# Performance work log

Measured on AMD Instinct MI355X. Metric: run time of the kernel, lower is better.

## Reference

```python
import jax, jax.numpy as jnp
import numpy as np

B, S, D, H, L, F = 2, 2048, 512, 8, 6, 2048
MAX = 5000
HD = D // H
OFF = MAX - 1


def _layernorm(x, g, b, eps=1e-5):
    m = jnp.mean(x, axis=-1, keepdims=True)
    v = jnp.mean((x - m) ** 2, axis=-1, keepdims=True)
    return (x - m) / jnp.sqrt(v + eps) * g + b


def _sinusoidal_pe(seq_len, d_model):
    pos = jnp.arange(seq_len, dtype=jnp.float32)[:, None]
    div = jnp.exp(jnp.arange(0, d_model, 2, dtype=jnp.float32) * (-np.log(10000.0) / d_model))
    pe = jnp.zeros((seq_len, d_model), jnp.float32)
    pe = pe.at[:, 0::2].set(jnp.sin(pos * div))
    pe = pe.at[:, 1::2].set(jnp.cos(pos * div))
    return pe


def setup_inputs() -> dict:
    key = jax.random.key(0)
    ks = iter(jax.random.split(key, 64))

    def n(shape, s):
        return (jax.random.normal(next(ks), shape, jnp.float32) * s).astype(jnp.float32)

    inp = {}
    inp['x'] = jax.random.normal(next(ks), (B, S, D), jnp.float32)
    inp['f0'] = jax.random.normal(next(ks), (B, S, 1), jnp.float32)
    inp['sp'] = jax.random.normal(next(ks), (B, S, 1), jnp.float32)
    inp['ap'] = jax.random.normal(next(ks), (B, S, 1), jnp.float32)
    inp['spk_emb'] = jax.random.normal(next(ks), (B, D), jnp.float32)
    # conditional positional encoding projections (weights stored as (in,out); y = x @ W + b)
    inp['Wf0'] = n((1, D), 0.1); inp['bf0'] = jnp.zeros((D,), jnp.float32)
    inp['Wsp'] = n((1, D), 0.1); inp['bsp'] = jnp.zeros((D,), jnp.float32)
    inp['Wap'] = n((1, D), 0.1); inp['bap'] = jnp.zeros((D,), jnp.float32)
    inp['Wspk'] = n((D, D), 0.02); inp['bspk'] = jnp.zeros((D,), jnp.float32)
    # per-layer stacked params
    inp['Wq'] = n((L, D, D), 0.02); inp['bq'] = jnp.zeros((L, D), jnp.float32)
    inp['Wk'] = n((L, D, D), 0.02); inp['bk'] = jnp.zeros((L, D), jnp.float32)
    inp['Wv'] = n((L, D, D), 0.02); inp['bv'] = jnp.zeros((L, D), jnp.float32)
    inp['Wo'] = n((L, D, D), 0.02); inp['bo'] = jnp.zeros((L, D), jnp.float32)
    inp['ln1_g'] = jnp.ones((L, D), jnp.float32); inp['ln1_b'] = jnp.zeros((L, D), jnp.float32)
    inp['ln2_g'] = jnp.ones((L, D), jnp.float32); inp['ln2_b'] = jnp.zeros((L, D), jnp.float32)
    inp['W1'] = n((L, D, F), 0.02); inp['b1'] = jnp.zeros((L, F), jnp.float32)
    inp['W2'] = n((L, F, D), 0.02); inp['b2'] = jnp.zeros((L, D), jnp.float32)
    inp['rel_table'] = n((L, 2 * MAX - 1, H), 0.02)
    inp['gfin'] = jnp.ones((D,), jnp.float32); inp['bfin'] = jnp.zeros((D,), jnp.float32)
    return inp


def _forward(x, f0, sp, ap, spk_emb,
             Wf0, bf0, Wsp, bsp, Wap, bap, Wspk, bspk,
             Wq, bq, Wk, bk, Wv, bv, Wo, bo,
             ln1_g, ln1_b, ln2_g, ln2_b, W1, b1, W2, b2,
             rel_table, gfin, bfin):
    # --- conditional positional encoding (dropout = identity, eval mode) ---
    x = x + _sinusoidal_pe(S, D)[None]
    x = x + (f0 @ Wf0 + bf0)
    x = x + (sp @ Wsp + bsp)
    x = x + (ap @ Wap + bap)
    spk = jnp.broadcast_to(spk_emb[:, None, :], (B, S, D))
    x = x + (spk @ Wspk + bspk)

    # relative coords: added bias for (query q, key k) is table[k - q + OFF] (matches transpose(1,3) in torch)
    coords = jnp.arange(S)
    rel = jnp.clip(coords[None, :] - coords[:, None] + OFF, 0, 2 * MAX - 2)  # (S_q, S_k)

    scale = 1.0 / np.sqrt(HD)

    def layer(x, p):
        (Wq_, bq_, Wk_, bk_, Wv_, bv_, Wo_, bo_,
         g1, be1, g2, be2, W1_, b1_, W2_, b2_, tab) = p
        res = x
        h = _layernorm(x, g1, be1)
        Q = (h @ Wq_ + bq_).reshape(B, S, H, HD)
        K = (h @ Wk_ + bk_).reshape(B, S, H, HD)
        V = (h @ Wv_ + bv_).reshape(B, S, H, HD)
        scores = jnp.einsum('bqhd,bkhd->bhqk', Q, K) * scale
        bias = jnp.transpose(tab[rel], (2, 0, 1))  # (H, S_q, S_k)
        scores = scores + bias[None]
        attn = jax.nn.softmax(scores, axis=-1)
        ao = jnp.einsum('bhqk,bkhd->bqhd', attn, V).reshape(B, S, D)
        x = res + (ao @ Wo_ + bo_)
        res = x
        h = _layernorm(x, g2, be2)
        h = jax.nn.gelu(h @ W1_ + b1_, approximate=False)
        x = res + (h @ W2_ + b2_)
        return x, None

    params = (Wq, bq, Wk, bk, Wv, bv, Wo, bo,
              ln1_g, ln1_b, ln2_g, ln2_b, W1, b1, W2, b2, rel_table)
    x, _ = jax.lax.scan(layer, x, params)
    return _layernorm(x, gfin, bfin)


def reference(x, f0, sp, ap, spk_emb,
              Wf0, bf0, Wsp, bsp, Wap, bap, Wspk, bspk,
              Wq, bq, Wk, bk, Wv, bv, Wo, bo,
              ln1_g, ln1_b, ln2_g, ln2_b, W1, b1, W2, b2,
              rel_table, gfin, bfin):
    return _forward(x, f0, sp, ap, spk_emb,
                    Wf0, bf0, Wsp, bsp, Wap, bap, Wspk, bspk,
                    Wq, bq, Wk, bk, Wv, bv, Wo, bo,
                    ln1_g, ln1_b, ln2_g, ln2_b, W1, b1, W2, b2,
                    rel_table, gfin, bfin)
```

## Files before the change

kernel.cpp:

```cpp
#include <hip/hip_runtime.h>
#include <hip/hip_bf16.h>

#define B_ 2
#define S_ 2048
#define D_ 512
#define H_ 8
#define L_ 6
#define F_ 2048
#define HD_ 64
#define M_ 4096
#define OFF_ 4999
#define NREL_ 9999

typedef short s8v __attribute__((ext_vector_type(8)));
typedef float f4v __attribute__((ext_vector_type(4)));

enum { MODE_BF16 = 0, MODE_RES = 1, MODE_GELU = 2 };

__device__ __forceinline__ short f2bf(float f) {
  unsigned u = __float_as_uint(f);
  unsigned r = (u + 0x7fffu + ((u >> 16) & 1u)) >> 16;
  return (short)r;
}

__device__ __forceinline__ float exp2fast(float x) {
  float r;
  asm("v_exp_f32 %0, %1" : "=v"(r) : "v"(x));
  return r;
}

__device__ __forceinline__ void gload16(const void* g, const void* l) {
  __builtin_amdgcn_global_load_lds((const __attribute__((address_space(1))) unsigned int*)g,
                                   (__attribute__((address_space(3))) unsigned int*)l,
                                   16, 0, 0);
}

__global__ void transpose_kernel(const float* __restrict__ src, short* __restrict__ dst,
                                 int K, int N, long srcBS, long dstBS, int rowOff)
{
  __shared__ float t[32][33];
  int tx = threadIdx.x, ty = threadIdx.y;
  int n0 = blockIdx.x * 32, k0 = blockIdx.y * 32, l = blockIdx.z;
  const float* s = src + (size_t)l * srcBS;
  short* d = dst + (size_t)l * dstBS;
  for (int j = 0; j < 4; ++j)
    t[ty + j*8][tx] = s[(size_t)(k0 + ty + j*8) * N + n0 + tx];
  __syncthreads();
  for (int j = 0; j < 4; ++j)
    d[(size_t)(rowOff + n0 + ty + j*8) * K + k0 + tx] = f2bf(t[tx][ty + j*8]);
}

__global__ void packb_kernel(const float* __restrict__ bq, const float* __restrict__ bk,
                             const float* __restrict__ bv, float* __restrict__ bqkv)
{
  int i = blockIdx.x * 256 + threadIdx.x;
  if (i >= L_ * 1536) return;
  int l = i / 1536, j = i % 1536;
  float v = (j < 512) ? bq[l*512 + j] : (j < 1024) ? bk[l*512 + j - 512] : bv[l*512 + j - 1024];
  bqkv[i] = v;
}

__global__ void tabt_kernel(const float* __restrict__ tab, float* __restrict__ tabT)
{
  int i = blockIdx.x * 256 + threadIdx.x;
  if (i >= L_ * H_ * NREL_) return;
  int l = i / (H_ * NREL_), rem = i % (H_ * NREL_);
  int h = rem / NREL_, idx = rem % NREL_;
  tabT[i] = tab[((size_t)l * NREL_ + idx) * H_ + h] * 1.44269504f;
}

__global__ __launch_bounds__(256) void spk_kernel(const float* __restrict__ spk,
                                                  const float* __restrict__ Wspk,
                                                  const float* __restrict__ bspk,
                                                  float* __restrict__ sproj)
{
  __shared__ float red[4][64];
  int b = blockIdx.x, nb = blockIdx.y;
  int dl = threadIdx.x & 63, kc = threadIdx.x >> 6;
  int d = nb * 64 + dl;
  const float* sprow = spk + b * D_;
  float a0 = 0.f, a1 = 0.f;
  int kbeg = kc * 128;
  for (int k = kbeg; k < kbeg + 128; k += 2) {
    a0 += sprow[k]     * Wspk[(size_t)k * D_ + d];
    a1 += sprow[k + 1] * Wspk[(size_t)(k + 1) * D_ + d];
  }
  red[kc][dl] = a0 + a1;
  __syncthreads();
  if (kc == 0)
    sproj[b*D_ + d] = red[0][dl] + red[1][dl] + red[2][dl] + red[3][dl] + bspk[d];
}

__global__ __launch_bounds__(256) void prologue_kernel(
    const float* __restrict__ x, const float* __restrict__ f0, const float* __restrict__ sp,
    const float* __restrict__ ap, const float* __restrict__ Wf0, const float* __restrict__ bf0,
    const float* __restrict__ Wsp, const float* __restrict__ bsp,
    const float* __restrict__ Wap, const float* __restrict__ bap,
    const float* __restrict__ sproj, float* __restrict__ X)
{
  int row = blockIdx.x, tid = threadIdx.x;
  int b = row >> 11, s = row & 2047;
  float vf0 = f0[row], vsp = sp[row], vap = ap[row];
  for (int j = 0; j < 2; ++j) {
    int d = tid + j * 256;
    int i = d >> 1;
    float div = expf((float)(2*i) * -0.01798894603f);
    float arg = (float)s * div;
    float pe = (d & 1) ? cosf(arg) : sinf(arg);
    float v = x[(size_t)row*D_ + d] + pe
            + vf0*Wf0[d] + bf0[d] + vsp*Wsp[d] + bsp[d] + vap*Wap[d] + bap[d]
            + sproj[b*D_ + d];
    X[(size_t)row*D_ + d] = v;
  }
}

__global__ __launch_bounds__(256) void ln_kernel(
    const float* __restrict__ X, const float* __restrict__ g, const float* __restrict__ bta,
    short* __restrict__ outB, float* __restrict__ outF, int f32out)
{
  __shared__ float red[8];
  int row = blockIdx.x, tid = threadIdx.x;
  const float* xr = X + (size_t)row * D_;
  float v0 = xr[tid], v1 = xr[tid + 256];
  float s = v0 + v1, q = v0*v0 + v1*v1;
  for (int off = 1; off < 64; off <<= 1) { s += __shfl_xor(s, off); q += __shfl_xor(q, off); }
  int w = tid >> 6;
  if ((tid & 63) == 0) { red[w*2] = s; red[w*2 + 1] = q; }
  __syncthreads();
  s = red[0] + red[2] + red[4] + red[6];
  q = red[1] + red[3] + red[5] + red[7];
  float mean = s * (1.0f / D_);
  float var = q * (1.0f / D_) - mean * mean;
  float rstd = rsqrtf(var + 1e-5f);
  float o0 = (v0 - mean) * rstd * g[tid] + bta[tid];
  float o1 = (v1 - mean) * rstd * g[tid + 256] + bta[tid + 256];
  if (f32out) {
    outF[(size_t)row*D_ + tid] = o0; outF[(size_t)row*D_ + tid + 256] = o1;
  } else {
    outB[(size_t)row*D_ + tid] = f2bf(o0); outB[(size_t)row*D_ + tid + 256] = f2bf(o1);
  }
}

template<int MODE>
__device__ __forceinline__ void gemm_body(
    const short* __restrict__ A, const short* __restrict__ Wt,
    const float* __restrict__ bias, int K, int N,
    float* outF, short* outB)
{
  __shared__ short sA[2][4096];
  __shared__ short sB[2][2048];
  const int tid = threadIdx.x;
  const int w = tid >> 6, lane = tid & 63;
  const int col = lane & 15, quad = lane >> 4;
  const int m0 = blockIdx.x * 128, n0 = blockIdx.y * 64;
  const int z = blockIdx.z;
  const int Ksub = K / gridDim.z;
  const int kbase = z * Ksub;
  const int nkt = Ksub >> 6;

  const int rowT = tid >> 2, kcA = tid & 3;
  const size_t kc8 = kcA * 8;

  f4v acc[2][4] = {};
  for (int kt = 0; kt < nkt; ++kt) {
    const int k0 = kbase + kt * 64;
    __syncthreads();
    for (int p = 0; p < 2; ++p) {
      gload16(A + (size_t)(m0 + rowT) * K + k0 + p*32 + kc8,       &sA[p][(w*16) * 32]);
      gload16(A + (size_t)(m0 + 64 + rowT) * K + k0 + p*32 + kc8,  &sA[p][(64 + w*16) * 32]);
      gload16(Wt + (size_t)(n0 + rowT) * K + k0 + p*32 + kc8,      &sB[p][(w*16) * 32]);
    }
    __syncthreads();
    for (int p = 0; p < 2; ++p) {
      s8v af[2], bfr[4];
      for (int mt = 0; mt < 2; ++mt)
        af[mt] = *(const s8v*)&sA[p][(w*32 + mt*16 + col) * 32 + quad * 8];
      for (int nt = 0; nt < 4; ++nt)
        bfr[nt] = *(const s8v*)&sB[p][(nt*16 + col) * 32 + quad * 8];
      for (int mt = 0; mt < 2; ++mt)
        for (int nt = 0; nt < 4; ++nt)
          acc[mt][nt] = __builtin_amdgcn_mfma_f32_16x16x32_bf16(af[mt], bfr[nt], acc[mt][nt], 0, 0, 0);
    }
  }

  const float qsc = (MODE == MODE_BF16 && n0 < 512) ? 0.18033688f : 1.0f;
  float bz[4];
  for (int nt = 0; nt < 4; ++nt)
    bz[nt] = (z == 0) ? bias[n0 + nt*16 + col] : 0.0f;
  for (int mt = 0; mt < 2; ++mt) {
    int mbase = m0 + w*32 + mt*16 + quad*4;
    for (int nt = 0; nt < 4; ++nt) {
      int n = n0 + nt*16 + col;
      for (int r = 0; r < 4; ++r) {
        float v = acc[mt][nt][r] + bz[nt];
        size_t idx = (size_t)(mbase + r) * N + n;
        if (MODE == MODE_RES) {
          atomicAdd(outF + idx, v);
        } else if (MODE == MODE_GELU) {
          outB[idx] = f2bf(0.5f * v * (1.0f + erff(v * 0.70710678118f)));
        } else {
          outB[idx] = f2bf(v * qsc);
        }
      }
    }
  }
}

__global__ __launch_bounds__(256) void gemm_qkv_kernel(
    const short* __restrict__ A, const short* __restrict__ Wt,
    const float* __restrict__ bias, float* outF, short* outB)
{ gemm_body<MODE_BF16>(A, Wt, bias, 512, 1536, outF, outB); }

__global__ __launch_bounds__(256) void gemm_o_kernel(
    const short* __restrict__ A, const short* __restrict__ Wt,
    const float* __restrict__ bias, float* outF, short* outB)
{ gemm_body<MODE_RES>(A, Wt, bias, 512, 512, outF, outB); }

__global__ __launch_bounds__(256) void gemm_ffn1_kernel(
    const short* __restrict__ A, const short* __restrict__ Wt,
    const float* __restrict__ bias, float* outF, short* outB)
{ gemm_body<MODE_GELU>(A, Wt, bias, 512, 2048, outF, outB); }

__global__ __launch_bounds__(256) void gemm_ffn2_kernel(
    const short* __restrict__ A, const short* __restrict__ Wt,
    const float* __restrict__ bias, float* outF, short* outB)
{ gemm_body<MODE_RES>(A, Wt, bias, 2048, 512, outF, outB); }

__global__ __launch_bounds__(256) void vtrans_kernel(const short* __restrict__ QKV,
                                                     short* __restrict__ Vt)
{
  __shared__ short t[64 * 72];
  int tid = threadIdx.x;
  int s0 = blockIdx.x * 64, bh = blockIdx.y;
  int b = bh >> 3, h = bh & 7;
  for (int it = 0; it < 2; ++it) {
    int c = it * 256 + tid;
    int sR = c >> 3, hc = c & 7;
    s8v v = *(const s8v*)(QKV + (size_t)(b*S_ + s0 + sR) * 1536 + 1024 + h*64 + hc*8);
    *(s8v*)&t[sR * 72 + hc * 8] = v;
  }
  __syncthreads();
  for (int it = 0; it < 2; ++it) {
    int c = it * 256 + tid;
    int hd = c >> 3, sc = c & 7;
    s8v v;
    for (int j = 0; j < 8; ++j) v[j] = t[(sc*8 + j) * 72 + hd];
    *(s8v*)(Vt + (size_t)(bh*64 + hd) * S_ + s0 + sc*8) = v;
  }
}

__global__ __launch_bounds__(512) void flash_kernel(
    const short* __restrict__ QKV, const short* __restrict__ Vt,
    const float* __restrict__ tabT, short* __restrict__ AO)
{
  __shared__ __attribute__((aligned(16))) short sQ[2 * 128 * 40];
  __shared__ __attribute__((aligned(16))) short sK[2 * 2 * 32 * 40];
  __shared__ __attribute__((aligned(16))) short sV[2 * 64 * 40];
  __shared__ __attribute__((aligned(16))) short sP[8 * 2 * 16 * 40];
  __shared__ float sBias[192];
  __shared__ float sRow[8 * 16];

  const int tid = threadIdx.x;
  const int w = tid >> 6, lane = tid & 63;
  const int col = lane & 15, quad = lane >> 4;
  const int bh = blockIdx.x, qt = blockIdx.y;
  const int b = bh >> 3, h = bh & 7;
  const int q0 = qt * 128;
  const int wq = w * 16;
  const int nkt = S_ / 64;
  const float* tabh = tabT + (size_t)h * NREL_;

  for (int j = 0; j < 2; ++j) {
    int Lc = j * 512 + tid;
    int c4q = Lc & 3, q = (Lc >> 2) & 127, hc = Lc >> 9;
    *(int4*)&sQ[hc*5120 + q*40 + c4q*8] =
      *(const int4*)(QKV + (size_t)(b*S_ + q0 + q) * 1536 + h*64 + hc*32 + c4q*8);
  }

  const int c4 = tid & 3;
  const int kK = (tid >> 2) & 63, hcK = tid >> 8;
  const short* gK = QKV + (size_t)(b*S_ + kK) * 1536 + 512 + h*64 + hcK*32 + c4*8;
  short* dK = &sK[(kK >> 5)*2560 + hcK*1280 + (kK & 31)*40 + c4*8];
  const int c8 = tid & 7, hdV = tid >> 3;
  const short* gV = Vt + (size_t)(bh*64 + hdV) * S_ + c8*8;
  short* dV = &sV[(c8 >> 2)*2560 + hdV*40 + (c8 & 3)*8];

  int4 rk = *(const int4*)gK;
  int4 rv = *(const int4*)gV;
  float rbias = (tid < 192) ? tabh[0 - q0 - 127 + OFF_ + tid] : 0.0f;

  s8v bQ[2];
  float lsum = 0.0f;
  f4v o[4] = {};

  for (int kt = 0; kt < nkt; ++kt) {
    __syncthreads();
    *(int4*)dK = rk;
    *(int4*)dV = rv;
    if (tid < 192) sBias[tid] = rbias;
    __syncthreads();
    if (kt == 0) {
      bQ[0] = *(const s8v*)&sQ[0*5120 + (wq + col)*40 + quad*8];
      bQ[1] = *(const s8v*)&sQ[1*5120 + (wq + col)*40 + quad*8];
    }
    if (kt + 1 < nkt) {
      rk = *(const int4*)(gK + (size_t)(kt + 1) * 64 * 1536);
      rv = *(const int4*)(gV + (kt + 1) * 64);
      if (tid < 192) rbias = tabh[(kt + 1)*64 - q0 - 127 + OFF_ + tid];
    }

    for (int ko = 0; ko < 2; ++ko) {
      f4v st[2] = {};
      for (int mt = 0; mt < 2; ++mt) {
        s8v aK0 = *(const s8v*)&sK[ko*2560 + 0*1280 + (mt*16 + col)*40 + quad*8];
        s8v aK1 = *(const s8v*)&sK[ko*2560 + 1*1280 + (mt*16 + col)*40 + quad*8];
        st[mt] = __builtin_amdgcn_mfma_f32_16x16x32_bf16(aK0, bQ[0], st[mt], 0, 0, 0);
        st[mt] = __builtin_amdgcn_mfma_f32_16x16x32_bf16(aK1, bQ[1], st[mt], 0, 0, 0);
      }
      for (int mt = 0; mt < 2; ++mt) {
        int ib0 = ko*32 + mt*16 + quad*4 + 127 - wq - col;
        float p0 = exp2fast(st[mt][0] + sBias[ib0 + 0]);
        float p1 = exp2fast(st[mt][1] + sBias[ib0 + 1]);
        float p2 = exp2fast(st[mt][2] + sBias[ib0 + 2]);
        float p3 = exp2fast(st[mt][3] + sBias[ib0 + 3]);
        lsum += (p0 + p1) + (p2 + p3);
        unsigned u0 = __float_as_uint(p0) + 0x8000u;
        unsigned u1 = __float_as_uint(p1) + 0x8000u;
        unsigned u2 = __float_as_uint(p2) + 0x8000u;
        unsigned u3 = __float_as_uint(p3) + 0x8000u;
        int2 pk;
        pk.x = (int)((u0 >> 16) | (u1 & 0xffff0000u));
        pk.y = (int)((u2 >> 16) | (u3 & 0xffff0000u));
        *(int2*)&sP[w*1280 + ko*640 + col*40 + mt*16 + quad*4] = pk;
      }
      s8v aP = *(const s8v*)&sP[w*1280 + ko*640 + col*40 + quad*8];
      for (int nt = 0; nt < 4; ++nt) {
        s8v bv = *(const s8v*)&sV[ko*2560 + (nt*16 + col)*40 + quad*8];
        o[nt] = __builtin_amdgcn_mfma_f32_16x16x32_bf16(aP, bv, o[nt], 0, 0, 0);
      }
    }
  }

  lsum += __shfl_xor(lsum, 16);
  lsum += __shfl_xor(lsum, 32);
  if (lane < 16) sRow[w*16 + lane] = lsum;
  float rs[4];
  for (int r = 0; r < 4; ++r) rs[r] = sRow[w*16 + quad*4 + r];
  for (int nt = 0; nt < 4; ++nt)
    for (int r = 0; r < 4; ++r) {
      float v = o[nt][r] / rs[r];
      size_t m = (size_t)(b*S_ + q0 + wq + quad*4 + r);
      AO[m * 512 + h*64 + nt*16 + col] = f2bf(v);
    }
}

extern "C" void kernel_launch(void* const* d_in, const int* in_sizes, int n_in,
                              void* d_out, int out_size, void* d_ws, size_t ws_size,
                              hipStream_t stream)
{
  const float* x    = (const float*)d_in[0];
  const float* f0   = (const float*)d_in[1];
  const float* sp   = (const float*)d_in[2];
  const float* ap   = (const float*)d_in[3];
  const float* spk  = (const float*)d_in[4];
  const float* Wf0  = (const float*)d_in[5];  const float* bf0  = (const float*)d_in[6];
  const float* Wsp  = (const float*)d_in[7];  const float* bsp  = (const float*)d_in[8];
  const float* Wap  = (const float*)d_in[9];  const float* bap  = (const float*)d_in[10];
  const float* Wspk = (const float*)d_in[11]; const float* bspk = (const float*)d_in[12];
  const float* Wq   = (const float*)d_in[13]; const float* bq   = (const float*)d_in[14];
  const float* Wk   = (const float*)d_in[15]; const float* bk   = (const float*)d_in[16];
  const float* Wv   = (const float*)d_in[17]; const float* bv   = (const float*)d_in[18];
  const float* Wo   = (const float*)d_in[19]; const float* bo   = (const float*)d_in[20];
  const float* ln1g = (const float*)d_in[21]; const float* ln1b = (const float*)d_in[22];
  const float* ln2g = (const float*)d_in[23]; const float* ln2b = (const float*)d_in[24];
  const float* W1   = (const float*)d_in[25]; const float* b1   = (const float*)d_in[26];
  const float* W2   = (const float*)d_in[27]; const float* b2   = (const float*)d_in[28];
  const float* tab  = (const float*)d_in[29];
  const float* gfin = (const float*)d_in[30]; const float* bfin = (const float*)d_in[31];

  char* p = (char*)d_ws;
  auto alloc = [&](size_t bytes) { char* r = p; p += (bytes + 255) & ~(size_t)255; return r; };
  short* WqkvT = (short*)alloc((size_t)L_ * 1536 * 512 * 2);
  short* WoT   = (short*)alloc((size_t)L_ * 512 * 512 * 2);
  short* W1T   = (short*)alloc((size_t)L_ * 2048 * 512 * 2);
  short* W2T   = (short*)alloc((size_t)L_ * 512 * 2048 * 2);
  float* bqkv  = (float*)alloc((size_t)L_ * 1536 * 4);
  float* X     = (float*)alloc((size_t)M_ * D_ * 4);
  short* Hb    = (short*)alloc((size_t)M_ * D_ * 2);
  short* AO    = (short*)alloc((size_t)M_ * D_ * 2);
  short* QKVb  = (short*)alloc((size_t)M_ * 1536 * 2);
  short* VtG   = (short*)alloc((size_t)B_ * H_ * HD_ * S_ * 2);
  short* H1b   = QKVb;
  float* sproj = (float*)alloc((size_t)B_ * D_ * 4);
  float* tabT  = (float*)alloc((size_t)L_ * H_ * NREL_ * 4);

  dim3 b256(256);
  dim3 tb(32, 8);
  packb_kernel<<<dim3((L_*1536 + 255)/256), b256, 0, stream>>>(bq, bk, bv, bqkv);
  tabt_kernel<<<dim3((L_*H_*NREL_ + 255)/256), b256, 0, stream>>>(tab, tabT);
  transpose_kernel<<<dim3(16, 16, L_), tb, 0, stream>>>(Wq, WqkvT, 512, 512, 512*512, 1536*512, 0);
  transpose_kernel<<<dim3(16, 16, L_), tb, 0, stream>>>(Wk, WqkvT, 512, 512, 512*512, 1536*512, 512);
  transpose_kernel<<<dim3(16, 16, L_), tb, 0, stream>>>(Wv, WqkvT, 512, 512, 512*512, 1536*512, 1024);
  transpose_kernel<<<dim3(16, 16, L_), tb, 0, stream>>>(Wo, WoT, 512, 512, 512*512, 512*512, 0);
  transpose_kernel<<<dim3(64, 16, L_), tb, 0, stream>>>(W1, W1T, 512, 2048, 512*2048, 2048*512, 0);
  transpose_kernel<<<dim3(16, 64, L_), tb, 0, stream>>>(W2, W2T, 2048, 512, 2048*512, 512*2048, 0);
  spk_kernel<<<dim3(B_, 8), b256, 0, stream>>>(spk, Wspk, bspk, sproj);
  prologue_kernel<<<dim3(M_), b256, 0, stream>>>(x, f0, sp, ap, Wf0, bf0, Wsp, bsp, Wap, bap, sproj, X);

  for (int l = 0; l < L_; ++l) {
    ln_kernel<<<dim3(M_), b256, 0, stream>>>(X, ln1g + l*D_, ln1b + l*D_, Hb, nullptr, 0);
    gemm_qkv_kernel<<<dim3(32, 24, 1), b256, 0, stream>>>(
        Hb, WqkvT + (size_t)l*1536*512, bqkv + l*1536, nullptr, QKVb);
    vtrans_kernel<<<dim3(S_/64, B_*H_), b256, 0, stream>>>(QKVb, VtG);
    flash_kernel<<<dim3(B_*H_, S_/128), dim3(512), 0, stream>>>(QKVb, VtG, tabT + (size_t)l*H_*NREL_, AO);
    gemm_o_kernel<<<dim3(32, 8, 2), b256, 0, stream>>>(
        AO, WoT + (size_t)l*512*512, bo + l*D_, X, nullptr);
    ln_kernel<<<dim3(M_), b256, 0, stream>>>(X, ln2g + l*D_, ln2b + l*D_, Hb, nullptr, 0);
    gemm_ffn1_kernel<<<dim3(32, 32, 1), b256, 0, stream>>>(
        Hb, W1T + (size_t)l*2048*512, b1 + l*F_, nullptr, H1b);
    gemm_ffn2_kernel<<<dim3(32, 8, 4), b256, 0, stream>>>(
        H1b, W2T + (size_t)l*512*2048, b2 + l*D_, X, nullptr);
  }
  ln_kernel<<<dim3(M_), b256, 0, stream>>>(X, gfin, bfin, nullptr, (float*)d_out, 1);
}
```

Before: 1.019 ms.

## Split flash attention over key ranges with atomic partial accumulation

Splits the attention key loop three ways across a new grid dimension so more blocks run concurrently. Partial outputs and row sums are combined with float atomics into zeroed fp32 buffers, then a new normalize kernel divides and converts to bf16. It also reads Q straight from global memory instead of staging it in LDS, and packs P to bf16 with a hardware convert instruction. The trade is an extra zeroing kernel, an extra normalize pass and atomic traffic. This relies on softmax without max subtraction, so the partial sums can simply be added.

After: 1.113 ms. 1.09x slower.

```diff
diff --git a/kernel.cpp b/kernel.cpp
--- a/kernel.cpp
+++ b/kernel.cpp
@@ -29,10 +29,22 @@
   return r;
 }
 
+__device__ __forceinline__ int cvt_pk_bf16(float lo, float hi) {
+  int r;
+  asm("v_cvt_pk_bf16_f32 %0, %1, %2" : "=v"(r) : "v"(lo), "v"(hi));
+  return r;
+}
+
 __device__ __forceinline__ void gload16(const void* g, const void* l) {
   __builtin_amdgcn_global_load_lds((const __attribute__((address_space(1))) unsigned int*)g,
                                    (__attribute__((address_space(3))) unsigned int*)l,
                                    16, 0, 0);
+}
+
+__global__ __launch_bounds__(256) void zero_kernel(float* __restrict__ dst)
+{
+  size_t i = ((size_t)blockIdx.x * 256 + threadIdx.x) * 4;
+  *(float4*)(dst + i) = make_float4(0.f, 0.f, 0.f, 0.f);
 }
 
 __global__ void transpose_kernel(const float* __restrict__ src, short* __restrict__ dst,
@@ -249,33 +261,31 @@
   }
 }
 
-__global__ __launch_bounds__(512) void flash_kernel(
+__global__ __launch_bounds__(512, 6) void flash_kernel(
     const short* __restrict__ QKV, const short* __restrict__ Vt,
-    const float* __restrict__ tabT, short* __restrict__ AO)
-{
-  __shared__ __attribute__((aligned(16))) short sQ[2 * 128 * 40];
+    const float* __restrict__ tabT, float* __restrict__ Oacc, float* __restrict__ Lsum)
+{
   __shared__ __attribute__((aligned(16))) short sK[2 * 2 * 32 * 40];
   __shared__ __attribute__((aligned(16))) short sV[2 * 64 * 40];
   __shared__ __attribute__((aligned(16))) short sP[8 * 2 * 16 * 40];
   __shared__ float sBias[192];
-  __shared__ float sRow[8 * 16];
 
   const int tid = threadIdx.x;
   const int w = tid >> 6, lane = tid & 63;
   const int col = lane & 15, quad = lane >> 4;
-  const int bh = blockIdx.x, qt = blockIdx.y;
+  const int bh = blockIdx.x, qt = blockIdx.y, z = blockIdx.z;
   const int b = bh >> 3, h = bh & 7;
   const int q0 = qt * 128;
   const int wq = w * 16;
-  const int nkt = S_ / 64;
   const float* tabh = tabT + (size_t)h * NREL_;
 
-  for (int j = 0; j < 2; ++j) {
-    int Lc = j * 512 + tid;
-    int c4q = Lc & 3, q = (Lc >> 2) & 127, hc = Lc >> 9;
-    *(int4*)&sQ[hc*5120 + q*40 + c4q*8] =
-      *(const int4*)(QKV + (size_t)(b*S_ + q0 + q) * 1536 + h*64 + hc*32 + c4q*8);
-  }
+  const int ktBeg = (z == 0) ? 0 : (z == 1) ? 11 : 22;
+  const int ktEnd = (z == 0) ? 11 : (z == 1) ? 22 : 32;
+
+  const short* gQ = QKV + (size_t)(b*S_ + q0 + wq + col) * 1536 + h*64 + quad*8;
+  s8v bQ[2];
+  bQ[0] = *(const s8v*)gQ;
+  bQ[1] = *(const s8v*)(gQ + 32);
 
   const int c4 = tid & 3;
   const int kK = (tid >> 2) & 63, hcK = tid >> 8;
@@ -285,25 +295,20 @@
   const short* gV = Vt + (size_t)(bh*64 + hdV) * S_ + c8*8;
   short* dV = &sV[(c8 >> 2)*2560 + hdV*40 + (c8 & 3)*8];
 
-  int4 rk = *(const int4*)gK;
-  int4 rv = *(const int4*)gV;
-  float rbias = (tid < 192) ? tabh[0 - q0 - 127 + OFF_ + tid] : 0.0f;
-
-  s8v bQ[2];
+  int4 rk = *(const int4*)(gK + (size_t)ktBeg * 64 * 1536);
+  int4 rv = *(const int4*)(gV + ktBeg * 64);
+  float rbias = (tid < 192) ? tabh[ktBeg*64 - q0 - 127 + OFF_ + tid] : 0.0f;
+
   float lsum = 0.0f;
   f4v o[4] = {};
 
-  for (int kt = 0; kt < nkt; ++kt) {
+  for (int kt = ktBeg; kt < ktEnd; ++kt) {
     __syncthreads();
     *(int4*)dK = rk;
     *(int4*)dV = rv;
     if (tid < 192) sBias[tid] = rbias;
     __syncthreads();
-    if (kt == 0) {
-      bQ[0] = *(const s8v*)&sQ[0*5120 + (wq + col)*40 + quad*8];
-      bQ[1] = *(const s8v*)&sQ[1*5120 + (wq + col)*40 + quad*8];
-    }
-    if (kt + 1 < nkt) {
+    if (kt + 1 < ktEnd) {
       rk = *(const int4*)(gK + (size_t)(kt + 1) * 64 * 1536);
       rv = *(const int4*)(gV + (kt + 1) * 64);
       if (tid < 192) rbias = tabh[(kt + 1)*64 - q0 - 127 + OFF_ + tid];
@@ -324,13 +329,9 @@
         float p2 = exp2fast(st[mt][2] + sBias[ib0 + 2]);
         float p3 = exp2fast(st[mt][3] + sBias[ib0 + 3]);
         lsum += (p0 + p1) + (p2 + p3);
-        unsigned u0 = __float_as_uint(p0) + 0x8000u;
-        unsigned u1 = __float_as_uint(p1) + 0x8000u;
-        unsigned u2 = __float_as_uint(p2) + 0x8000u;
-        unsigned u3 = __float_as_uint(p3) + 0x8000u;
         int2 pk;
-        pk.x = (int)((u0 >> 16) | (u1 & 0xffff0000u));
-        pk.y = (int)((u2 >> 16) | (u3 & 0xffff0000u));
+        pk.x = cvt_pk_bf16(p0, p1);
+        pk.y = cvt_pk_bf16(p2, p3);
         *(int2*)&sP[w*1280 + ko*640 + col*40 + mt*16 + quad*4] = pk;
       }
       s8v aP = *(const s8v*)&sP[w*1280 + ko*640 + col*40 + quad*8];
@@ -343,15 +344,27 @@
 
   lsum += __shfl_xor(lsum, 16);
   lsum += __shfl_xor(lsum, 32);
-  if (lane < 16) sRow[w*16 + lane] = lsum;
-  float rs[4];
-  for (int r = 0; r < 4; ++r) rs[r] = sRow[w*16 + quad*4 + r];
+  if (lane < 16)
+    atomicAdd(&Lsum[(size_t)bh * S_ + q0 + wq + lane], lsum);
   for (int nt = 0; nt < 4; ++nt)
     for (int r = 0; r < 4; ++r) {
-      float v = o[nt][r] / rs[r];
       size_t m = (size_t)(b*S_ + q0 + wq + quad*4 + r);
-      AO[m * 512 + h*64 + nt*16 + col] = f2bf(v);
-    }
+      atomicAdd(&Oacc[m * 512 + h*64 + nt*16 + col], o[nt][r]);
+    }
+}
+
+__global__ __launch_bounds__(256) void attn_norm_kernel(
+    const float* __restrict__ Oacc, const float* __restrict__ Ls, short* __restrict__ AO)
+{
+  int row = blockIdx.x, tid = threadIdx.x;
+  int b = row >> 11, s = row & 2047;
+  const float* orow = Oacc + (size_t)row * D_;
+  short* arow = AO + (size_t)row * D_;
+  for (int j = 0; j < 2; ++j) {
+    int c = tid + j * 256;
+    int h = c >> 6;
+    arow[c] = f2bf(orow[c] / Ls[(size_t)(b*8 + h) * S_ + s]);
+  }
 }
 
 extern "C" void kernel_launch(void* const* d_in, const int* in_sizes, int n_in,
@@ -393,6 +406,8 @@
   short* H1b   = QKVb;
   float* sproj = (float*)alloc((size_t)B_ * D_ * 4);
   float* tabT  = (float*)alloc((size_t)L_ * H_ * NREL_ * 4);
+  float* Oacc  = (float*)alloc((size_t)M_ * D_ * 4);
+  float* Lsum  = (float*)alloc((size_t)B_ * H_ * S_ * 4);
 
   dim3 b256(256);
   dim3 tb(32, 8);
@@ -407,12 +422,16 @@
   spk_kernel<<<dim3(B_, 8), b256, 0, stream>>>(spk, Wspk, bspk, sproj);
   prologue_kernel<<<dim3(M_), b256, 0, stream>>>(x, f0, sp, ap, Wf0, bf0, Wsp, bsp, Wap, bap, sproj, X);
 
+  const int zeroBlocks = (int)(((size_t)M_ * D_ * 4 + (size_t)B_ * H_ * S_ * 4) / 16 / 256);
   for (int l = 0; l < L_; ++l) {
     ln_kernel<<<dim3(M_), b256, 0, stream>>>(X, ln1g + l*D_, ln1b + l*D_, Hb, nullptr, 0);
     gemm_qkv_kernel<<<dim3(32, 24, 1), b256, 0, stream>>>(
         Hb, WqkvT + (size_t)l*1536*512, bqkv + l*1536, nullptr, QKVb);
     vtrans_kernel<<<dim3(S_/64, B_*H_), b256, 0, stream>>>(QKVb, VtG);
-    flash_kernel<<<dim3(B_*H_, S_/128), dim3(512), 0, stream>>>(QKVb, VtG, tabT + (size_t)l*H_*NREL_, AO);
+    zero_kernel<<<dim3(zeroBlocks), b256, 0, stream>>>(Oacc);
+    flash_kernel<<<dim3(B_*H_, S_/128, 3), dim3(512), 0, stream>>>(
+        QKVb, VtG, tabT + (size_t)l*H_*NREL_, Oacc, Lsum);
+    attn_norm_kernel<<<dim3(M_), b256, 0, stream>>>(Oacc, Lsum, AO);
     gemm_o_kernel<<<dim3(32, 8, 2), b256, 0, stream>>>(
         AO, WoT + (size_t)l*512*512, bo + l*D_, X, nullptr);
     ln_kernel<<<dim3(M_), b256, 0, stream>>>(X, ln2g + l*D_, ln2b + l*D_, Hb, nullptr, 0);
```

## Load Q and K fragments directly from global into registers in flash kernel

Applied to the files above, without the earlier changes.

Removes the shared-memory staging of Q and K in the flash attention kernel. Each wave now loads its Q fragment and the K MFMA operand fragments straight from global memory into registers, double-buffering K across iterations with an unrolled two-step loop. The P conversion uses the hardware packed bf16 convert instruction, and launch bounds request two blocks per CU. In exchange this raises register pressure, and each wave issues redundant global loads of K, since every wave now fetches the full K tile instead of sharing it through LDS.

After: 1.174 ms. 1.15x slower.

```diff
diff --git a/kernel.cpp b/kernel.cpp
--- a/kernel.cpp
+++ b/kernel.cpp
@@ -26,6 +26,12 @@
 __device__ __forceinline__ float exp2fast(float x) {
   float r;
   asm("v_exp_f32 %0, %1" : "=v"(r) : "v"(x));
+  return r;
+}
+
+__device__ __forceinline__ int cvt_pk_bf16(float lo, float hi) {
+  int r;
+  asm("v_cvt_pk_bf16_f32 %0, %1, %2" : "=v"(r) : "v"(lo), "v"(hi));
   return r;
 }
 
@@ -249,12 +255,10 @@
   }
 }
 
-__global__ __launch_bounds__(512) void flash_kernel(
+__global__ __launch_bounds__(512, 2) void flash_kernel(
     const short* __restrict__ QKV, const short* __restrict__ Vt,
     const float* __restrict__ tabT, short* __restrict__ AO)
 {
-  __shared__ __attribute__((aligned(16))) short sQ[2 * 128 * 40];
-  __shared__ __attribute__((aligned(16))) short sK[2 * 2 * 32 * 40];
   __shared__ __attribute__((aligned(16))) short sV[2 * 64 * 40];
   __shared__ __attribute__((aligned(16))) short sP[8 * 2 * 16 * 40];
   __shared__ float sBias[192];
@@ -270,53 +274,52 @@
   const int nkt = S_ / 64;
   const float* tabh = tabT + (size_t)h * NREL_;
 
-  for (int j = 0; j < 2; ++j) {
-    int Lc = j * 512 + tid;
-    int c4q = Lc & 3, q = (Lc >> 2) & 127, hc = Lc >> 9;
-    *(int4*)&sQ[hc*5120 + q*40 + c4q*8] =
-      *(const int4*)(QKV + (size_t)(b*S_ + q0 + q) * 1536 + h*64 + hc*32 + c4q*8);
-  }
-
-  const int c4 = tid & 3;
-  const int kK = (tid >> 2) & 63, hcK = tid >> 8;
-  const short* gK = QKV + (size_t)(b*S_ + kK) * 1536 + 512 + h*64 + hcK*32 + c4*8;
-  short* dK = &sK[(kK >> 5)*2560 + hcK*1280 + (kK & 31)*40 + c4*8];
+  const short* gQ = QKV + (size_t)(b*S_ + q0 + wq + col) * 1536 + h*64 + quad*8;
+  s8v bQ[2];
+  bQ[0] = *(const s8v*)gQ;
+  bQ[1] = *(const s8v*)(gQ + 32);
+
   const int c8 = tid & 7, hdV = tid >> 3;
   const short* gV = Vt + (size_t)(bh*64 + hdV) * S_ + c8*8;
   short* dV = &sV[(c8 >> 2)*2560 + hdV*40 + (c8 & 3)*8];
 
-  int4 rk = *(const int4*)gK;
+  const short* gKf = QKV + (size_t)(b*S_ + col) * 1536 + 512 + h*64 + quad*8;
+  s8v kf0[8], kf1[8];
+  auto loadK = [&](s8v* dst, int ktv) {
+    const short* gk = gKf + (size_t)ktv * 64 * 1536;
+    #pragma unroll
+    for (int i = 0; i < 8; ++i) {
+      const int ko = i >> 2, mt = (i >> 1) & 1, hc = i & 1;
+      dst[i] = *(const s8v*)(gk + (size_t)(ko*32 + mt*16) * 1536 + hc*32);
+    }
+  };
+
   int4 rv = *(const int4*)gV;
   float rbias = (tid < 192) ? tabh[0 - q0 - 127 + OFF_ + tid] : 0.0f;
-
-  s8v bQ[2];
+  loadK(kf0, 0);
+
   float lsum = 0.0f;
   f4v o[4] = {};
 
-  for (int kt = 0; kt < nkt; ++kt) {
+  auto step = [&](int kt, s8v* cur, s8v* nxt) {
     __syncthreads();
-    *(int4*)dK = rk;
     *(int4*)dV = rv;
     if (tid < 192) sBias[tid] = rbias;
     __syncthreads();
-    if (kt == 0) {
-      bQ[0] = *(const s8v*)&sQ[0*5120 + (wq + col)*40 + quad*8];
-      bQ[1] = *(const s8v*)&sQ[1*5120 + (wq + col)*40 + quad*8];
-    }
-    if (kt + 1 < nkt) {
-      rk = *(const int4*)(gK + (size_t)(kt + 1) * 64 * 1536);
-      rv = *(const int4*)(gV + (kt + 1) * 64);
-      if (tid < 192) rbias = tabh[(kt + 1)*64 - q0 - 127 + OFF_ + tid];
-    }
-
+    const int ktn = (kt + 1 < nkt) ? kt + 1 : nkt - 1;
+    rv = *(const int4*)(gV + ktn * 64);
+    if (tid < 192) rbias = tabh[ktn*64 - q0 - 127 + OFF_ + tid];
+    loadK(nxt, ktn);
+
+    #pragma unroll
     for (int ko = 0; ko < 2; ++ko) {
       f4v st[2] = {};
+      #pragma unroll
       for (int mt = 0; mt < 2; ++mt) {
-        s8v aK0 = *(const s8v*)&sK[ko*2560 + 0*1280 + (mt*16 + col)*40 + quad*8];
-        s8v aK1 = *(const s8v*)&sK[ko*2560 + 1*1280 + (mt*16 + col)*40 + quad*8];
-        st[mt] = __builtin_amdgcn_mfma_f32_16x16x32_bf16(aK0, bQ[0], st[mt], 0, 0, 0);
-        st[mt] = __builtin_amdgcn_mfma_f32_16x16x32_bf16(aK1, bQ[1], st[mt], 0, 0, 0);
+        st[mt] = __builtin_amdgcn_mfma_f32_16x16x32_bf16(cur[ko*4 + mt*2 + 0], bQ[0], st[mt], 0, 0, 0);
+        st[mt] = __builtin_amdgcn_mfma_f32_16x16x32_bf16(cur[ko*4 + mt*2 + 1], bQ[1], st[mt], 0, 0, 0);
       }
+      #pragma unroll
       for (int mt = 0; mt < 2; ++mt) {
         int ib0 = ko*32 + mt*16 + quad*4 + 127 - wq - col;
         float p0 = exp2fast(st[mt][0] + sBias[ib0 + 0]);
@@ -324,21 +327,23 @@
         float p2 = exp2fast(st[mt][2] + sBias[ib0 + 2]);
         float p3 = exp2fast(st[mt][3] + sBias[ib0 + 3]);
         lsum += (p0 + p1) + (p2 + p3);
-        unsigned u0 = __float_as_uint(p0) + 0x8000u;
-        unsigned u1 = __float_as_uint(p1) + 0x8000u;
-        unsigned u2 = __float_as_uint(p2) + 0x8000u;
-        unsigned u3 = __float_as_uint(p3) + 0x8000u;
         int2 pk;
-        pk.x = (int)((u0 >> 16) | (u1 & 0xffff0000u));
-        pk.y = (int)((u2 >> 16) | (u3 & 0xffff0000u));
+        pk.x = cvt_pk_bf16(p0, p1);
+        pk.y = cvt_pk_bf16(p2, p3);
         *(int2*)&sP[w*1280 + ko*640 + col*40 + mt*16 + quad*4] = pk;
       }
       s8v aP = *(const s8v*)&sP[w*1280 + ko*640 + col*40 + quad*8];
+      #pragma unroll
       for (int nt = 0; nt < 4; ++nt) {
         s8v bv = *(const s8v*)&sV[ko*2560 + (nt*16 + col)*40 + quad*8];
         o[nt] = __builtin_amdgcn_mfma_f32_16x16x32_bf16(aP, bv, o[nt], 0, 0, 0);
       }
     }
+  };
+
+  for (int kt = 0; kt < nkt; kt += 2) {
+    step(kt,     kf0, kf1);
+    step(kt + 1, kf1, kf0);
   }
 
   lsum += __shfl_xor(lsum, 16);
```
